# Optimization experiments

Hardware: AMD Instinct MI355X
Metric: run time of the kernel (lower is better)

The kernel has to match this reference:

```python
import jax, jax.numpy as jnp
import numpy as np
import math

N_HEADS = 16
LN_EPS = 1e-5


def _layernorm(x, scale, bias):
    mu = jnp.mean(x, axis=-1, keepdims=True)
    var = jnp.var(x, axis=-1, keepdims=True)
    return (x - mu) * jax.lax.rsqrt(var + LN_EPS) * scale + bias


def _pos_encoding(seq_len, d_model, dtype):
    pos = jnp.arange(seq_len, dtype=jnp.float32)[:, None]
    div = jnp.exp(jnp.arange(0, d_model, 2, dtype=jnp.float32) * (-math.log(10000.0) / d_model))
    pe = jnp.zeros((seq_len, d_model), dtype=jnp.float32)
    pe = pe.at[:, 0::2].set(jnp.sin(pos * div))
    pe = pe.at[:, 1::2].set(jnp.cos(pos * div))
    return pe.astype(dtype)


def setup_inputs() -> dict:
    key = jax.random.key(0)
    ks = jax.random.split(key, 8)
    B, S, V, D, L = 2, 1024, 32000, 1024, 6
    F = 4 * D
    sc = 0.02
    return {
        "tokens": jax.random.randint(ks[0], (B, S), 0, V, dtype=jnp.int32),
        "token_emb": jax.random.normal(ks[1], (V, D), jnp.float32) * sc,
        "Wqkv": jax.random.normal(ks[2], (L, D, 3 * D), jnp.float32) * sc,
        "Wout": jax.random.normal(ks[3], (L, D, D), jnp.float32) * sc,
        "ln1_s": jnp.ones((L, D), jnp.float32),
        "ln1_b": jnp.zeros((L, D), jnp.float32),
        "W1": jax.random.normal(ks[4], (L, D, F), jnp.float32) * sc,
        "b1": jnp.zeros((L, F), jnp.float32),
        "W2": jax.random.normal(ks[5], (L, F, D), jnp.float32) * sc,
        "b2": jnp.zeros((L, D), jnp.float32),
        "ln2_s": jnp.ones((L, D), jnp.float32),
        "ln2_b": jnp.zeros((L, D), jnp.float32),
        "lnf_s": jnp.ones((D,), jnp.float32),
        "lnf_b": jnp.zeros((D,), jnp.float32),
        "Whead": jax.random.normal(ks[6], (D, V), jnp.float32) * sc,
        "bhead": jnp.zeros((V,), jnp.float32),
    }


def _forward(tokens, token_emb, Wqkv, Wout, ln1_s, ln1_b, W1, b1, W2, b2,
             ln2_s, ln2_b, lnf_s, lnf_b, Whead, bhead):
    B, S = tokens.shape
    D = token_emb.shape[1]
    L = Wqkv.shape[0]
    H = N_HEADS
    dk = D // H

    x = token_emb[tokens] + _pos_encoding(S, D, token_emb.dtype)  # [B,S,D]
    causal = jnp.tril(jnp.ones((S, S), dtype=bool))
    neg_inf = jnp.finfo(x.dtype).min

    for l in range(L):
        # --- attention sublayer ---
        h = _layernorm(x, ln1_s[l], ln1_b[l])
        qkv = (h @ Wqkv[l]).reshape(B, S, 3, H, dk)
        q, k, v = jnp.moveaxis(qkv, 2, 0)  # each [B,S,H,dk]
        scores = jnp.einsum('bqhd,bkhd->bhqk', q, k) / math.sqrt(dk)
        scores = jnp.where(causal, scores, neg_inf)
        attn = jax.nn.softmax(scores, axis=-1)  # [B,H,S,S]
        o = jnp.einsum('bhqk,bkhd->bqhd', attn, v).reshape(B, S, D)
        x = x + o @ Wout[l]
        # --- FFN sublayer ---
        h2 = _layernorm(x, ln2_s[l], ln2_b[l])
        x = x + jax.nn.gelu(h2 @ W1[l] + b1[l], approximate=False) @ W2[l] + b2[l]

    x = _layernorm(x, lnf_s, lnf_b)
    return x @ Whead + bhead  # [B,S,V]


def reference(tokens, token_emb, Wqkv, Wout, ln1_s, ln1_b, W1, b1, W2, b2,
              ln2_s, ln2_b, lnf_s, lnf_b, Whead, bhead):
    return _forward(tokens, token_emb, Wqkv, Wout, ln1_s, ln1_b, W1, b1, W2, b2,
                    ln2_s, ln2_b, lnf_s, lnf_b, Whead, bhead)
```

## Files before the change

kernel.cpp:

```cpp
#include <hip/hip_runtime.h>
#include <hip/hip_bf16.h>
#include <math.h>

typedef __bf16 bf16;
typedef __bf16 bf16x8 __attribute__((ext_vector_type(8)));
typedef float f32x4 __attribute__((ext_vector_type(4)));

#define GL_AS(p) ((const __attribute__((address_space(1))) void*)(p))
#define LDS_AS(p) ((__attribute__((address_space(3))) void*)(p))

__global__ __launch_bounds__(256) void transpose_cast_k(
    const float* __restrict__ in, bf16* __restrict__ out, int R, int C)
{
    __shared__ float t[32][33];
    const int c0 = blockIdx.x * 32, r0 = blockIdx.y * 32;
    const size_t zoff = (size_t)blockIdx.z * R * C;
    const float* inb = in + zoff;
    bf16* outb = out + zoff;
    const int tx = threadIdx.x, ty = threadIdx.y;
#pragma unroll
    for (int i = 0; i < 32; i += 8)
        t[ty + i][tx] = inb[(size_t)(r0 + ty + i) * C + c0 + tx];
    __syncthreads();
#pragma unroll
    for (int i = 0; i < 32; i += 8)
        outb[(size_t)(c0 + ty + i) * R + r0 + tx] = (bf16)t[tx][ty + i];
}

__global__ __launch_bounds__(256) void embed_k(
    const int* __restrict__ tok, const float* __restrict__ emb,
    float* __restrict__ x)
{
    const int D = 1024;
    const int row = blockIdx.x;
    const int s = row & 1023;
    const int t = tok[row];
#pragma unroll
    for (int i = 0; i < 4; ++i) {
        const int d = threadIdx.x + i * 256;
        const int half = d >> 1;
        const float div = expf(-(float)half * (9.210340371976184f / 512.0f));
        const float ang = (float)s * div;
        const float pe = (d & 1) ? cosf(ang) : sinf(ang);
        x[(size_t)row * D + d] = emb[(size_t)t * D + d] + pe;
    }
}

__global__ __launch_bounds__(256) void layernorm_k(
    const float* __restrict__ x, const float* __restrict__ sc,
    const float* __restrict__ bi, bf16* __restrict__ out)
{
    const int D = 1024;
    const int row = blockIdx.x;
    const float* xr = x + (size_t)row * D;
    float vals[4];
    float s = 0.f, q = 0.f;
#pragma unroll
    for (int i = 0; i < 4; ++i) {
        const float v = xr[threadIdx.x + i * 256];
        vals[i] = v; s += v; q += v * v;
    }
#pragma unroll
    for (int o = 32; o; o >>= 1) { s += __shfl_xor(s, o); q += __shfl_xor(q, o); }
    __shared__ float ls[4], lq[4];
    const int w = threadIdx.x >> 6;
    if ((threadIdx.x & 63) == 0) { ls[w] = s; lq[w] = q; }
    __syncthreads();
    const float S = ls[0] + ls[1] + ls[2] + ls[3];
    const float Q = lq[0] + lq[1] + lq[2] + lq[3];
    const float mu = S * (1.0f / D);
    const float var = Q * (1.0f / D) - mu * mu;
    const float rstd = rsqrtf(var + 1e-5f);
#pragma unroll
    for (int i = 0; i < 4; ++i) {
        const int d = threadIdx.x + i * 256;
        out[(size_t)row * D + d] = (bf16)((vals[i] - mu) * rstd * sc[d] + bi[d]);
    }
}

template <int EPI, int SK = 1>
__global__ __launch_bounds__(256, 2) void gemm_bt_k(
    const bf16* __restrict__ A, const bf16* __restrict__ Bt,
    float* __restrict__ Cf, bf16* __restrict__ Cb, bf16* __restrict__ Cb2,
    const float* __restrict__ bias, int M, int N, int K)
{
    __shared__ __align__(16) bf16 Al[128 * 64];
    __shared__ __align__(16) bf16 Bl[128 * 64];
    const int tid = threadIdx.x;
    const int l = tid & 63;
    const int wbase = tid & 192;
    const int wr = (tid >> 7) & 1, wc = (tid >> 6) & 1;
    const int bm = blockIdx.x, bn = blockIdx.y;
    const int kz = blockIdx.z;
    const int Kc = K / SK;

    f32x4 acc[4][4];
#pragma unroll
    for (int i = 0; i < 4; ++i)
#pragma unroll
        for (int j = 0; j < 4; ++j) acc[i][j] = (f32x4){0.f, 0.f, 0.f, 0.f};

    const bf16* Abase = A + (size_t)bm * 128 * K + (size_t)kz * Kc;
    const bf16* Bbase = Bt + (size_t)bn * 128 * K + (size_t)kz * Kc;

    for (int k0 = 0; k0 < Kc; k0 += 64) {
#pragma unroll
        for (int i = 0; i < 4; ++i) {
            const int c = i * 256 + tid;
            const int row = c >> 3, slot = c & 7;
            const int col = ((slot ^ (row & 7)) << 3);
            __builtin_amdgcn_global_load_lds(
                GL_AS(Abase + (size_t)row * K + k0 + col),
                LDS_AS(Al + (i * 256 + wbase) * 8), 16, 0, 0);
        }
#pragma unroll
        for (int i = 0; i < 4; ++i) {
            const int c = i * 256 + tid;
            const int row = c >> 3, slot = c & 7;
            const int col = ((slot ^ (row & 7)) << 3);
            __builtin_amdgcn_global_load_lds(
                GL_AS(Bbase + (size_t)row * K + k0 + col),
                LDS_AS(Bl + (i * 256 + wbase) * 8), 16, 0, 0);
        }
        __syncthreads();

#pragma unroll
        for (int ks = 0; ks < 2; ++ks) {
            bf16x8 af[4], bfr[4];
            const int kb = ks * 64 + ((l >> 4) << 4);
#pragma unroll
            for (int mi = 0; mi < 4; ++mi) {
                const int r = wr * 64 + mi * 16 + (l & 15);
                af[mi] = *(const bf16x8*)((const char*)Al + r * 128 + (kb ^ ((r & 7) << 4)));
            }
#pragma unroll
            for (int ni = 0; ni < 4; ++ni) {
                const int r = wc * 64 + ni * 16 + (l & 15);
                bfr[ni] = *(const bf16x8*)((const char*)Bl + r * 128 + (kb ^ ((r & 7) << 4)));
            }
#pragma unroll
            for (int mi = 0; mi < 4; ++mi)
#pragma unroll
                for (int ni = 0; ni < 4; ++ni)
                    acc[mi][ni] = __builtin_amdgcn_mfma_f32_16x16x32_bf16(
                        af[mi], bfr[ni], acc[mi][ni], 0, 0, 0);
        }
        __syncthreads();
    }

    const int colb = bn * 128 + wc * 64;
    const int rowb = bm * 128 + wr * 64 + ((l >> 4) << 2);
#pragma unroll
    for (int mi = 0; mi < 4; ++mi) {
#pragma unroll
        for (int ni = 0; ni < 4; ++ni) {
            const int col = colb + ni * 16 + (l & 15);
#pragma unroll
            for (int j = 0; j < 4; ++j) {
                const int row = rowb + mi * 16 + j;
                const float v = acc[mi][ni][j];
                if constexpr (EPI == 0) {
                    Cb[(size_t)row * N + col] = (bf16)v;
                } else if constexpr (EPI == 1) {
                    if constexpr (SK > 1) atomicAdd(&Cf[(size_t)row * N + col], v);
                    else                  Cf[(size_t)row * N + col] += v;
                } else if constexpr (EPI == 2) {
                    const float u = v + bias[col];
                    const float g = 0.5f * u * (1.0f + erff(u * 0.70710678118654752f));
                    Cb[(size_t)row * N + col] = (bf16)g;
                } else if constexpr (EPI == 3) {
                    const float add = (SK == 1 || kz == 0) ? v + bias[col] : v;
                    if constexpr (SK > 1) atomicAdd(&Cf[(size_t)row * N + col], add);
                    else                  Cf[(size_t)row * N + col] += add;
                } else if constexpr (EPI == 4) {
                    __builtin_nontemporal_store(v + bias[col], &Cf[(size_t)row * N + col]);
                } else {
                    if (col < 2048) {
                        Cb[(size_t)row * N + col] = (bf16)v;
                    } else {
                        Cb2[((size_t)(row & ~1023) + (col - 2048)) * 1024 + (row & 1023)] = (bf16)v;
                    }
                }
            }
        }
    }
}

__global__ __launch_bounds__(256) void attn_mfma_k(
    const bf16* __restrict__ qkv, const bf16* __restrict__ vt,
    bf16* __restrict__ o)
{
    __shared__ __align__(16) bf16 Kl[2][32 * 64];
    __shared__ __align__(16) bf16 Vl[2][64 * 32];
    __shared__ __align__(16) bf16 Pl[4][16][88];

    const int tid = threadIdx.x;
    const int w = tid >> 6, l = tid & 63;
    const int g = l >> 4, lc = l & 15;
    const int qt = blockIdx.x & 15;
    const int bh = blockIdx.x >> 4;
    const int h = bh & 15, b = bh >> 4;
    const int q0 = qt * 64;
    const int qw = q0 + w * 16;
    const int diag = qw >> 5;
    const int NT = (q0 >> 5) + 2;

    const bf16* qbase = qkv + (size_t)b * 1024 * 3072 + h * 64;
    const bf16* kbase = qbase + 1024;
    const bf16* vbase = vt + (size_t)(b * 16 + h) * 64 * 1024;

    bf16x8 af0, af1;
    {
        const bf16* qp = qbase + (size_t)(qw + lc) * 3072 + g * 8;
        af0 = *(const bf16x8*)qp;
        af1 = *(const bf16x8*)(qp + 32);
    }

    f32x4 acc[4];
#pragma unroll
    for (int dt = 0; dt < 4; ++dt) acc[dt] = (f32x4){0.f, 0.f, 0.f, 0.f};
    f32x4 m  = (f32x4){-1e30f, -1e30f, -1e30f, -1e30f};
    f32x4 ls = (f32x4){0.f, 0.f, 0.f, 0.f};

    auto stage = [&](int t) {
        const int k0 = t * 32;
        const int buf = t & 1;
        {
            const int row = tid >> 3;
            const int d = (((tid & 7) ^ (row & 7)) << 3);
            __builtin_amdgcn_global_load_lds(
                GL_AS(kbase + (size_t)(k0 + row) * 3072 + d),
                LDS_AS(Kl[buf] + (tid & 192) * 8), 16, 0, 0);
        }
        {
            const int row = tid >> 2;
            const int s = (((tid & 3) ^ ((tid >> 3) & 3)) << 3);
            __builtin_amdgcn_global_load_lds(
                GL_AS(vbase + (size_t)row * 1024 + k0 + s),
                LDS_AS(Vl[buf] + (tid & 192) * 8), 16, 0, 0);
        }
    };

    auto compute = [&](int t, bool MASKED) {
        const char* KT = (const char*)Kl[t & 1];
        const char* VT = (const char*)Vl[t & 1];
        const int k0 = t * 32;

        const int r0 = lc, r1 = 16 + lc;
        const bf16x8 kf00 = *(const bf16x8*)(KT + r0 * 128 + 16 * (g       ^ (r0 & 7)));
        const bf16x8 kf01 = *(const bf16x8*)(KT + r0 * 128 + 16 * ((4 + g) ^ (r0 & 7)));
        const bf16x8 kf10 = *(const bf16x8*)(KT + r1 * 128 + 16 * (g       ^ (r1 & 7)));
        const bf16x8 kf11 = *(const bf16x8*)(KT + r1 * 128 + 16 * ((4 + g) ^ (r1 & 7)));

        f32x4 s0 = (f32x4){0.f, 0.f, 0.f, 0.f};
        f32x4 s1 = (f32x4){0.f, 0.f, 0.f, 0.f};
        s0 = __builtin_amdgcn_mfma_f32_16x16x32_bf16(af0, kf00, s0, 0, 0, 0);
        s0 = __builtin_amdgcn_mfma_f32_16x16x32_bf16(af1, kf01, s0, 0, 0, 0);
        s1 = __builtin_amdgcn_mfma_f32_16x16x32_bf16(af0, kf10, s1, 0, 0, 0);
        s1 = __builtin_amdgcn_mfma_f32_16x16x32_bf16(af1, kf11, s1, 0, 0, 0);

#pragma unroll
        for (int j = 0; j < 4; ++j) {
            if (MASKED) {
                const int row = qw + 4 * g + j;
                s0[j] = (k0 + lc <= row)      ? s0[j] * 0.125f : -1e30f;
                s1[j] = (k0 + 16 + lc <= row) ? s1[j] * 0.125f : -1e30f;
            } else {
                s0[j] *= 0.125f;
                s1[j] *= 0.125f;
            }
        }

        f32x4 tmx;
#pragma unroll
        for (int j = 0; j < 4; ++j) tmx[j] = fmaxf(s0[j], s1[j]);
#pragma unroll
        for (int off = 8; off; off >>= 1)
#pragma unroll
            for (int j = 0; j < 4; ++j) tmx[j] = fmaxf(tmx[j], __shfl_xor(tmx[j], off));

        f32x4 sc, p0, p1;
#pragma unroll
        for (int j = 0; j < 4; ++j) {
            const float mn = fmaxf(m[j], tmx[j]);
            sc[j] = __expf(m[j] - mn);
            p0[j] = __expf(s0[j] - mn);
            p1[j] = __expf(s1[j] - mn);
            m[j] = mn;
            ls[j] = ls[j] * sc[j] + p0[j] + p1[j];
        }
#pragma unroll
        for (int dt = 0; dt < 4; ++dt)
#pragma unroll
            for (int j = 0; j < 4; ++j) acc[dt][j] *= sc[j];

#pragma unroll
        for (int j = 0; j < 4; ++j) {
            const int r = 4 * g + j;
            const bf16 h0 = (bf16)p0[j];
            const bf16 h1 = (bf16)p1[j];
            Pl[w][r][lc]      = h0;
            Pl[w][r][16 + lc] = h1;
            Pl[w][r][48 + lc] = (bf16)(p0[j] - (float)h0);
            Pl[w][r][64 + lc] = (bf16)(p1[j] - (float)h1);
        }
        const bf16x8 pah = *(const bf16x8*)&Pl[w][lc][g * 8];
        const bf16x8 pal = *(const bf16x8*)&Pl[w][lc][48 + g * 8];

#pragma unroll
        for (int dt = 0; dt < 4; ++dt) {
            const int vr = dt * 16 + lc;
            const bf16x8 vf = *(const bf16x8*)(VT + vr * 64 + 16 * (g ^ ((vr >> 1) & 3)));
            acc[dt] = __builtin_amdgcn_mfma_f32_16x16x32_bf16(pah, vf, acc[dt], 0, 0, 0);
            acc[dt] = __builtin_amdgcn_mfma_f32_16x16x32_bf16(pal, vf, acc[dt], 0, 0, 0);
        }
    };

    stage(0);
    __syncthreads();
    for (int t = 0; t < NT; ++t) {
        if (t + 1 < NT) stage(t + 1);
        if (t <= diag) compute(t, t == diag);
        __syncthreads();
    }

    f32x4 inv;
#pragma unroll
    for (int j = 0; j < 4; ++j) {
        float s = ls[j];
#pragma unroll
        for (int off = 8; off; off >>= 1) s += __shfl_xor(s, off);
        inv[j] = 1.0f / s;
    }
    bf16* op = o + (size_t)(b * 1024 + qw) * 1024 + h * 64;
#pragma unroll
    for (int dt = 0; dt < 4; ++dt)
#pragma unroll
        for (int j = 0; j < 4; ++j)
            op[(size_t)(4 * g + j) * 1024 + dt * 16 + lc] = (bf16)(acc[dt][j] * inv[j]);
}

extern "C" void kernel_launch(void* const* d_in, const int* in_sizes, int n_in,
                              void* d_out, int out_size, void* d_ws, size_t ws_size,
                              hipStream_t stream)
{
    const int B = 2, S = 1024, D = 1024, L = 6, F = 4096, V = 32000, H = 16;
    const int M = B * S;

    const int*   tokens    = (const int*)  d_in[0];
    const float* token_emb = (const float*)d_in[1];
    const float* Wqkv      = (const float*)d_in[2];
    const float* Wout      = (const float*)d_in[3];
    const float* ln1_s     = (const float*)d_in[4];
    const float* ln1_b     = (const float*)d_in[5];
    const float* W1        = (const float*)d_in[6];
    const float* b1        = (const float*)d_in[7];
    const float* W2        = (const float*)d_in[8];
    const float* b2        = (const float*)d_in[9];
    const float* ln2_s     = (const float*)d_in[10];
    const float* ln2_b     = (const float*)d_in[11];
    const float* lnf_s     = (const float*)d_in[12];
    const float* lnf_b     = (const float*)d_in[13];
    const float* Whead     = (const float*)d_in[14];
    const float* bhead     = (const float*)d_in[15];
    float* out = (float*)d_out;

    char* w = (char*)d_ws;
    size_t off = 0;
    auto alloc = [&](size_t n) { char* p = w + off; off += (n + 255) & ~(size_t)255; return p; };
    bf16* WqkvT  = (bf16*)alloc((size_t)L * 3 * D * D * 2);
    bf16* WoutT  = (bf16*)alloc((size_t)L * D * D * 2);
    bf16* W1T    = (bf16*)alloc((size_t)L * F * D * 2);
    bf16* W2T    = (bf16*)alloc((size_t)L * D * F * 2);
    bf16* WheadT = (bf16*)alloc((size_t)V * D * 2);
    float* x     = (float*)alloc((size_t)M * D * 4);
    bf16* h      = (bf16*)alloc((size_t)M * D * 2);
    bf16* qkv    = (bf16*)alloc((size_t)M * 3 * D * 2);
    bf16* ob     = (bf16*)alloc((size_t)M * D * 2);
    bf16* mid    = (bf16*)alloc((size_t)M * F * 2);
    bf16* vt     = mid;

    const dim3 tb(32, 8);
    transpose_cast_k<<<dim3(3 * D / 32, D / 32, L), tb, 0, stream>>>(Wqkv, WqkvT, D, 3 * D);
    transpose_cast_k<<<dim3(D / 32, D / 32, L),     tb, 0, stream>>>(Wout, WoutT, D, D);
    transpose_cast_k<<<dim3(F / 32, D / 32, L),     tb, 0, stream>>>(W1, W1T, D, F);
    transpose_cast_k<<<dim3(D / 32, F / 32, L),     tb, 0, stream>>>(W2, W2T, F, D);
    transpose_cast_k<<<dim3(V / 32, D / 32, 1),     tb, 0, stream>>>(Whead, WheadT, D, V);

    embed_k<<<M, 256, 0, stream>>>(tokens, token_emb, x);

    for (int lyr = 0; lyr < L; ++lyr) {
        layernorm_k<<<M, 256, 0, stream>>>(x, ln1_s + lyr * D, ln1_b + lyr * D, h);
        gemm_bt_k<5><<<dim3(M / 128, 3 * D / 128), 256, 0, stream>>>(
            h, WqkvT + (size_t)lyr * 3 * D * D, nullptr, qkv, vt, nullptr, M, 3 * D, D);
        attn_mfma_k<<<B * H * S / 64, 256, 0, stream>>>(qkv, vt, ob);
        gemm_bt_k<1, 4><<<dim3(M / 128, D / 128, 4), 256, 0, stream>>>(
            ob, WoutT + (size_t)lyr * D * D, x, nullptr, nullptr, nullptr, M, D, D);
        layernorm_k<<<M, 256, 0, stream>>>(x, ln2_s + lyr * D, ln2_b + lyr * D, h);
        gemm_bt_k<2><<<dim3(M / 128, F / 128), 256, 0, stream>>>(
            h, W1T + (size_t)lyr * F * D, nullptr, mid, nullptr, b1 + lyr * F, M, F, D);
        gemm_bt_k<3, 4><<<dim3(M / 128, D / 128, 4), 256, 0, stream>>>(
            mid, W2T + (size_t)lyr * D * F, x, nullptr, nullptr, b2 + lyr * D, M, D, F);
    }
    layernorm_k<<<M, 256, 0, stream>>>(x, lnf_s, lnf_b, h);
    gemm_bt_k<4><<<dim3(M / 128, V / 128), 256, 0, stream>>>(
        h, WheadT, out, nullptr, nullptr, bhead, M, V, D);
}
```

Measured before the change: 1.582 ms.

## Fuse weight transposes, remap GEMM tiles across XCDs, vectorize LN/embed, retile V layout

The five weight transpose-cast launches become one kernel that walks segment descriptors. GEMM workgroups are remapped so neighbouring tiles land on the same XCD for L2 reuse. Layernorm and embedding use 4-wide vector loads and stores. The V-transpose output is reorganised into 8-row interleaved chunks so the QKV epilogue writes and the attention staging loads are more contiguous. The head GEMM store switches from nontemporal to a normal store. These are several independent changes, and the new V layout must match exactly between the GEMM epilogue and the attention loader.

```diff
diff --git a/kernel.cpp b/kernel.cpp
--- a/kernel.cpp
+++ b/kernel.cpp
@@ -3,28 +3,59 @@
 #include <math.h>
 
 typedef __bf16 bf16;
+typedef __bf16 bf16x4 __attribute__((ext_vector_type(4)));
 typedef __bf16 bf16x8 __attribute__((ext_vector_type(8)));
 typedef float f32x4 __attribute__((ext_vector_type(4)));
 
 #define GL_AS(p) ((const __attribute__((address_space(1))) void*)(p))
 #define LDS_AS(p) ((__attribute__((address_space(3))) void*)(p))
 
-__global__ __launch_bounds__(256) void transpose_cast_k(
-    const float* __restrict__ in, bf16* __restrict__ out, int R, int C)
-{
-    __shared__ float t[32][33];
-    const int c0 = blockIdx.x * 32, r0 = blockIdx.y * 32;
-    const size_t zoff = (size_t)blockIdx.z * R * C;
-    const float* inb = in + zoff;
-    bf16* outb = out + zoff;
+__device__ inline void xcd_remap(int& bm, int& bn, int NBM, int NBN)
+{
+    const int nwg = NBM * NBN;
+    const int flat = bm + NBM * bn;
+    const int q = nwg >> 3, r = nwg & 7;
+    const int x = flat & 7, i = flat >> 3;
+    const int f2 = ((x < r) ? x * (q + 1) : r * (q + 1) + (x - r) * q) + i;
+    bm = f2 % NBM;
+    bn = f2 / NBM;
+}
+
+struct TSeg {
+    const float* in; bf16* out; int R, C, nTilesC, tilesPerZ, nTiles;
+};
+
+__global__ __launch_bounds__(256) void transpose_all_k(
+    TSeg s0, TSeg s1, TSeg s2, TSeg s3, TSeg s4)
+{
+    int t = blockIdx.x;
+    TSeg s;
+    if (t < s0.nTiles) s = s0;
+    else { t -= s0.nTiles;
+    if (t < s1.nTiles) s = s1;
+    else { t -= s1.nTiles;
+    if (t < s2.nTiles) s = s2;
+    else { t -= s2.nTiles;
+    if (t < s3.nTiles) s = s3;
+    else { t -= s3.nTiles; s = s4; }}}}
+
+    const int z   = t / s.tilesPerZ;
+    const int rem = t - z * s.tilesPerZ;
+    const int cx  = rem % s.nTilesC, ry = rem / s.nTilesC;
+
+    __shared__ float tl[32][33];
+    const int c0 = cx * 32, r0 = ry * 32;
+    const size_t zoff = (size_t)z * s.R * s.C;
+    const float* inb = s.in + zoff;
+    bf16* outb = s.out + zoff;
     const int tx = threadIdx.x, ty = threadIdx.y;
 #pragma unroll
     for (int i = 0; i < 32; i += 8)
-        t[ty + i][tx] = inb[(size_t)(r0 + ty + i) * C + c0 + tx];
+        tl[ty + i][tx] = inb[(size_t)(r0 + ty + i) * s.C + c0 + tx];
     __syncthreads();
 #pragma unroll
     for (int i = 0; i < 32; i += 8)
-        outb[(size_t)(c0 + ty + i) * R + r0 + tx] = (bf16)t[tx][ty + i];
+        outb[(size_t)(c0 + ty + i) * s.R + r0 + tx] = (bf16)tl[tx][ty + i];
 }
 
 __global__ __launch_bounds__(256) void embed_k(
@@ -35,15 +66,18 @@
     const int row = blockIdx.x;
     const int s = row & 1023;
     const int t = tok[row];
-#pragma unroll
-    for (int i = 0; i < 4; ++i) {
-        const int d = threadIdx.x + i * 256;
-        const int half = d >> 1;
-        const float div = expf(-(float)half * (9.210340371976184f / 512.0f));
-        const float ang = (float)s * div;
-        const float pe = (d & 1) ? cosf(ang) : sinf(ang);
-        x[(size_t)row * D + d] = emb[(size_t)t * D + d] + pe;
-    }
+    const int d0 = threadIdx.x * 4;
+    const float c = 9.210340371976184f / 512.0f;
+    const float div0 = expf(-(float)(d0 >> 1) * c);
+    const float div1 = expf(-(float)((d0 >> 1) + 1) * c);
+    const float a0 = (float)s * div0, a1 = (float)s * div1;
+    const f32x4 e = *(const f32x4*)(emb + (size_t)t * D + d0);
+    f32x4 o;
+    o[0] = e[0] + sinf(a0);
+    o[1] = e[1] + cosf(a0);
+    o[2] = e[2] + sinf(a1);
+    o[3] = e[3] + cosf(a1);
+    *(f32x4*)(x + (size_t)row * D + d0) = o;
 }
 
 __global__ __launch_bounds__(256) void layernorm_k(
@@ -52,14 +86,10 @@
 {
     const int D = 1024;
     const int row = blockIdx.x;
-    const float* xr = x + (size_t)row * D;
-    float vals[4];
-    float s = 0.f, q = 0.f;
-#pragma unroll
-    for (int i = 0; i < 4; ++i) {
-        const float v = xr[threadIdx.x + i * 256];
-        vals[i] = v; s += v; q += v * v;
-    }
+    const int d0 = threadIdx.x * 4;
+    const f32x4 v = *(const f32x4*)(x + (size_t)row * D + d0);
+    float s = v[0] + v[1] + v[2] + v[3];
+    float q = v[0] * v[0] + v[1] * v[1] + v[2] * v[2] + v[3] * v[3];
 #pragma unroll
     for (int o = 32; o; o >>= 1) { s += __shfl_xor(s, o); q += __shfl_xor(q, o); }
     __shared__ float ls[4], lq[4];
@@ -71,11 +101,12 @@
     const float mu = S * (1.0f / D);
     const float var = Q * (1.0f / D) - mu * mu;
     const float rstd = rsqrtf(var + 1e-5f);
-#pragma unroll
-    for (int i = 0; i < 4; ++i) {
-        const int d = threadIdx.x + i * 256;
-        out[(size_t)row * D + d] = (bf16)((vals[i] - mu) * rstd * sc[d] + bi[d]);
-    }
+    const f32x4 sc4 = *(const f32x4*)(sc + d0);
+    const f32x4 bi4 = *(const f32x4*)(bi + d0);
+    bf16x4 o4;
+#pragma unroll
+    for (int i = 0; i < 4; ++i) o4[i] = (bf16)((v[i] - mu) * rstd * sc4[i] + bi4[i]);
+    *(bf16x4*)(out + (size_t)row * D + d0) = o4;
 }
 
 template <int EPI, int SK = 1>
@@ -90,7 +121,8 @@
     const int l = tid & 63;
     const int wbase = tid & 192;
     const int wr = (tid >> 7) & 1, wc = (tid >> 6) & 1;
-    const int bm = blockIdx.x, bn = blockIdx.y;
+    int bm = blockIdx.x, bn = blockIdx.y;
+    xcd_remap(bm, bn, gridDim.x, gridDim.y);
     const int kz = blockIdx.z;
     const int Kc = K / SK;
 
@@ -173,12 +205,12 @@
                     if constexpr (SK > 1) atomicAdd(&Cf[(size_t)row * N + col], add);
                     else                  Cf[(size_t)row * N + col] += add;
                 } else if constexpr (EPI == 4) {
-                    __builtin_nontemporal_store(v + bias[col], &Cf[(size_t)row * N + col]);
+                    Cf[(size_t)row * N + col] = v + bias[col];
                 } else {
                     if (col < 2048) {
                         Cb[(size_t)row * N + col] = (bf16)v;
                     } else {
-                        Cb2[((size_t)(row & ~1023) + (col - 2048)) * 1024 + (row & 1023)] = (bf16)v;
+                        Cb2[((size_t)(row >> 3) * 1024 + (col - 2048)) * 8 + (row & 7)] = (bf16)v;
                     }
                 }
             }
@@ -207,7 +239,7 @@
 
     const bf16* qbase = qkv + (size_t)b * 1024 * 3072 + h * 64;
     const bf16* kbase = qbase + 1024;
-    const bf16* vbase = vt + (size_t)(b * 16 + h) * 64 * 1024;
+    const bf16* vbase = vt + (size_t)b * 128 * 8192 + h * 64 * 8;
 
     bf16x8 af0, af1;
     {
@@ -234,9 +266,9 @@
         }
         {
             const int row = tid >> 2;
-            const int s = (((tid & 3) ^ ((tid >> 3) & 3)) << 3);
+            const int so = (tid & 3) ^ ((tid >> 3) & 3);
             __builtin_amdgcn_global_load_lds(
-                GL_AS(vbase + (size_t)row * 1024 + k0 + s),
+                GL_AS(vbase + (size_t)((k0 >> 3) + so) * 8192 + row * 8),
                 LDS_AS(Vl[buf] + (tid & 192) * 8), 16, 0, 0);
         }
     };
@@ -380,12 +412,13 @@
     bf16* mid    = (bf16*)alloc((size_t)M * F * 2);
     bf16* vt     = mid;
 
-    const dim3 tb(32, 8);
-    transpose_cast_k<<<dim3(3 * D / 32, D / 32, L), tb, 0, stream>>>(Wqkv, WqkvT, D, 3 * D);
-    transpose_cast_k<<<dim3(D / 32, D / 32, L),     tb, 0, stream>>>(Wout, WoutT, D, D);
-    transpose_cast_k<<<dim3(F / 32, D / 32, L),     tb, 0, stream>>>(W1, W1T, D, F);
-    transpose_cast_k<<<dim3(D / 32, F / 32, L),     tb, 0, stream>>>(W2, W2T, F, D);
-    transpose_cast_k<<<dim3(V / 32, D / 32, 1),     tb, 0, stream>>>(Whead, WheadT, D, V);
+    TSeg s0{Wqkv,  WqkvT,  D, 3 * D, 3 * D / 32, (3 * D / 32) * (D / 32), (3 * D / 32) * (D / 32) * L};
+    TSeg s1{Wout,  WoutT,  D, D,     D / 32,     (D / 32) * (D / 32),     (D / 32) * (D / 32) * L};
+    TSeg s2{W1,    W1T,    D, F,     F / 32,     (F / 32) * (D / 32),     (F / 32) * (D / 32) * L};
+    TSeg s3{W2,    W2T,    F, D,     D / 32,     (D / 32) * (F / 32),     (D / 32) * (F / 32) * L};
+    TSeg s4{Whead, WheadT, D, V,     V / 32,     (V / 32) * (D / 32),     (V / 32) * (D / 32)};
+    const int totTiles = s0.nTiles + s1.nTiles + s2.nTiles + s3.nTiles + s4.nTiles;
+    transpose_all_k<<<totTiles, dim3(32, 8), 0, stream>>>(s0, s1, s2, s3, s4);
 
     embed_k<<<M, 256, 0, stream>>>(tokens, token_emb, x);
 
```

Measured after the change: 1.595 ms. No clear change (+0.8%).
